# Performance work log

Hardware: AMD Instinct MI355X
Metric: run time of the kernel (lower is better)

Reference implementation:

```python
import jax, jax.numpy as jnp
import numpy as np

VOCAB, E, H, OUT = 24, 16, 32, 2
B, T = 16384, 128


def setup_inputs() -> dict:
    key = jax.random.key(0)
    ks = jax.random.split(key, 8)
    x = jax.random.randint(ks[0], (B, T), 0, VOCAB, dtype=jnp.int32)
    emb = jax.random.normal(ks[1], (VOCAB, E), dtype=jnp.float32) * 0.1
    emb = emb.at[0].set(0.0)  # padding_idx=0
    s = 1.0 / np.sqrt(H)
    W_ih = jax.random.uniform(ks[2], (4 * H, E), minval=-s, maxval=s, dtype=jnp.float32)
    W_hh = jax.random.uniform(ks[3], (4 * H, H), minval=-s, maxval=s, dtype=jnp.float32)
    b_ih = jax.random.uniform(ks[4], (4 * H,), minval=-s, maxval=s, dtype=jnp.float32)
    b_hh = jax.random.uniform(ks[5], (4 * H,), minval=-s, maxval=s, dtype=jnp.float32)
    sf = 1.0 / np.sqrt(H)
    fc_w = jax.random.uniform(ks[6], (OUT, H), minval=-sf, maxval=sf, dtype=jnp.float32)
    fc_b = jax.random.uniform(ks[7], (OUT,), minval=-sf, maxval=sf, dtype=jnp.float32)
    return {"x": x, "emb": emb, "W_ih": W_ih, "W_hh": W_hh,
            "b_ih": b_ih, "b_hh": b_hh, "fc_w": fc_w, "fc_b": fc_b}


def _lstm_last_h(xe, W_ih, W_hh, b_ih, b_hh):
    # xe: [B, T, E]. PyTorch gate order: i, f, g, o.
    b = xe.shape[0]
    # Precompute input projections for all timesteps in one GEMM: [B, T, 4H]
    gates_x = jnp.einsum('bte,ge->btg', xe, W_ih) + (b_ih + b_hh)

    def step(carry, gx_t):
        h, c = carry
        gates = gx_t + h @ W_hh.T  # [B, 4H]
        i, f, g, o = jnp.split(gates, 4, axis=-1)
        i = jax.nn.sigmoid(i)
        f = jax.nn.sigmoid(f)
        g = jnp.tanh(g)
        o = jax.nn.sigmoid(o)
        c = f * c + i * g
        h = o * jnp.tanh(c)
        return (h, c), None

    h0 = jnp.zeros((b, W_hh.shape[1]), dtype=xe.dtype)
    c0 = jnp.zeros_like(h0)
    (h_last, _), _ = jax.lax.scan(step, (h0, c0), jnp.swapaxes(gates_x, 0, 1))
    return h_last  # == lstm_outputs[:, -1, :]


def reference(x, emb, W_ih, W_hh, b_ih, b_hh, fc_w, fc_b):
    xe = emb[x]                                   # [B, T, E] embedding lookup
    h_last = _lstm_last_h(xe, W_ih, W_hh, b_ih, b_hh)  # [B, H]
    return h_last @ fc_w.T + fc_b                 # [B, 2]
```

## Files before the change

kernel.cpp:

```cpp
#include <hip/hip_runtime.h>
#include <hip/hip_bf16.h>

typedef __bf16 bf16x8 __attribute__((ext_vector_type(8)));
typedef float  f32x4  __attribute__((ext_vector_type(4)));

#define VOCAB 24
#define EDIM  16
#define HDIM  32
#define TLEN  128

union A2U { int4 w; bf16x8 v; };

__device__ __forceinline__ float rsig(float a) {
    return __builtin_amdgcn_rcpf(1.0f + __builtin_amdgcn_exp2f(a));
}
__device__ __forceinline__ float fast_tanh(float x) {
    float t = __builtin_amdgcn_exp2f(x * -2.88539008f);
    return fmaf(2.0f, __builtin_amdgcn_rcpf(1.0f + t), -1.0f);
}

__global__ __launch_bounds__(64) void lstm_fused(
    const int*   __restrict__ x,
    const float* __restrict__ emb,
    const float* __restrict__ W_ih,
    const float* __restrict__ W_hh,
    const float* __restrict__ b_ih,
    const float* __restrict__ b_hh,
    const float* __restrict__ fc_w,
    const float* __restrict__ fc_b,
    float*       __restrict__ out)
{
    __shared__ __align__(16) __bf16 hbuf[16][40];
    __shared__ __align__(16) float  fbuf[16][33];

    const int lane  = threadIdx.x;
    const int l15   = lane & 15;
    const int hi    = lane >> 4;
    const int kbase = hi * 8;
    const int kh    = hi * 4;
    const int row0  = blockIdx.x * 16;

    bf16x8 b1f[8];
    bf16x8 b2f[8];
    #pragma unroll
    for (int nt = 0; nt < 8; ++nt) {
        const int gcol = nt * 16 + l15;
        const float scale = ((nt >> 1) == 2) ? -2.88539008f : -1.44269504f;
        const float* wrow = W_hh + gcol * HDIM;
        #pragma unroll
        for (int i = 0; i < 8; ++i)
            b1f[nt][i] = (__bf16)(scale * wrow[kbase + i]);
        const float bias = b_ih[gcol] + b_hh[gcol];
        const float* wi = W_ih + gcol * EDIM;
        #pragma unroll
        for (int i = 0; i < 8; ++i) {
            const int v = kbase + i;
            float s = 0.0f;
            if (v < VOCAB) {
                s = bias;
                #pragma unroll
                for (int e = 0; e < EDIM; ++e)
                    s += emb[v * EDIM + e] * wi[e];
            }
            b2f[nt][i] = (__bf16)(scale * s);
        }
    }

    float c[8];
    #pragma unroll
    for (int q = 0; q < 8; ++q) c[q] = 0.0f;

    f32x4 p[8];
    f32x4 acc[8];
    const f32x4 z = {0.f, 0.f, 0.f, 0.f};
    const int* xrow = x + (row0 + l15) * TLEN;

#define PRECOMP(XV) do {                                                       \
    const int xv_   = (XV);                                                    \
    const int hotw_ = 0x3F80 << ((xv_ & 1) << 4);                              \
    const int hoth_ = xv_ >> 1;                                                \
    A2U a2_;                                                                   \
    a2_.w.x = (hoth_ == kh + 0) ? hotw_ : 0;                                   \
    a2_.w.y = (hoth_ == kh + 1) ? hotw_ : 0;                                   \
    a2_.w.z = (hoth_ == kh + 2) ? hotw_ : 0;                                   \
    a2_.w.w = (hoth_ == kh + 3) ? hotw_ : 0;                                   \
    _Pragma("unroll")                                                          \
    for (int nt = 0; nt < 8; ++nt)                                             \
        p[nt] = __builtin_amdgcn_mfma_f32_16x16x32_bf16(a2_.v, b2f[nt], z, 0, 0, 0); \
} while (0)

#define SLOT(FIRST, LAST, XVN) do {                                            \
    if (FIRST) {                                                               \
        _Pragma("unroll")                                                      \
        for (int nt = 0; nt < 8; ++nt) acc[nt] = p[nt];                        \
    } else {                                                                   \
        const bf16x8 a1_ = *(const bf16x8*)&hbuf[l15][kbase];                  \
        _Pragma("unroll")                                                      \
        for (int nt = 0; nt < 8; ++nt)                                         \
            acc[nt] = __builtin_amdgcn_mfma_f32_16x16x32_bf16(a1_, b1f[nt], p[nt], 0, 0, 0); \
    }                                                                          \
    if (!(LAST)) { PRECOMP(XVN); }        \
    _Pragma("unroll")                                                          \
    for (int qq = 0; qq < 2; ++qq) {                                           \
        _Pragma("unroll")                                                      \
        for (int r = 0; r < 4; ++r) {                                          \
            const float iv = rsig(acc[qq    ][r]);                             \
            const float fv = rsig(acc[qq + 2][r]);                             \
            const float gv = fmaf(2.0f, rsig(acc[qq + 4][r]), -1.0f);          \
            const float ov = rsig(acc[qq + 6][r]);                             \
            c[qq * 4 + r] = fmaf(fv, c[qq * 4 + r], iv * gv);                  \
            const float hv = ov * fast_tanh(c[qq * 4 + r]);                    \
            if (!(LAST)) hbuf[4 * hi + r][qq * 16 + l15] = (__bf16)hv;         \
            else         fbuf[4 * hi + r][qq * 16 + l15] = hv;                 \
        }                                                                      \
    }                                                                          \
} while (0)

    int4 q0 = *(const int4*)xrow;
    int4 xq = *(const int4*)(xrow + 4);
    PRECOMP(q0.x);

    SLOT(true,  false, q0.y);
    SLOT(false, false, q0.z);
    SLOT(false, false, q0.w);
    SLOT(false, false, xq.x);

    #pragma unroll 1
    for (int t = 4; t < 124; t += 4) {
        const int4 n = *(const int4*)(xrow + t + 4);
        SLOT(false, false, xq.y);
        SLOT(false, false, xq.z);
        SLOT(false, false, xq.w);
        SLOT(false, false, n.x);
        xq = n;
    }

    SLOT(false, false, xq.y);
    SLOT(false, false, xq.z);
    SLOT(false, false, xq.w);
    SLOT(false, true,  0);

#undef SLOT
#undef PRECOMP

    __syncthreads();

    if (lane < 16) {
        float o0 = fc_b[0], o1 = fc_b[1];
        #pragma unroll
        for (int jj = 0; jj < HDIM; ++jj) {
            const float h = fbuf[lane][jj];
            o0 += fc_w[jj]        * h;
            o1 += fc_w[HDIM + jj] * h;
        }
        float2 res;
        res.x = o0; res.y = o1;
        *(float2*)&out[(row0 + lane) * 2] = res;
    }
}

extern "C" void kernel_launch(void* const* d_in, const int* in_sizes, int n_in,
                              void* d_out, int out_size, void* d_ws, size_t ws_size,
                              hipStream_t stream) {
    const int*   x    = (const int*)  d_in[0];
    const float* emb  = (const float*)d_in[1];
    const float* W_ih = (const float*)d_in[2];
    const float* W_hh = (const float*)d_in[3];
    const float* b_ih = (const float*)d_in[4];
    const float* b_hh = (const float*)d_in[5];
    const float* fc_w = (const float*)d_in[6];
    const float* fc_b = (const float*)d_in[7];
    float* out = (float*)d_out;

    const int B    = in_sizes[0] / TLEN;
    const int nblk = B / 16;

    lstm_fused<<<nblk, 64, 0, stream>>>(x, emb, W_ih, W_hh, b_ih, b_hh, fc_w, fc_b, out);
}
```

Baseline: 110.1 us.

## Transpose MFMA operands and exchange hidden state via ds_bpermute instead of LDS

```diff
diff --git a/kernel.cpp b/kernel.cpp
--- a/kernel.cpp
+++ b/kernel.cpp
@@ -11,12 +11,12 @@
 
 union A2U { int4 w; bf16x8 v; };
 
-__device__ __forceinline__ float rsig(float a) {
-    return __builtin_amdgcn_rcpf(1.0f + __builtin_amdgcn_exp2f(a));
-}
-__device__ __forceinline__ float fast_tanh(float x) {
-    float t = __builtin_amdgcn_exp2f(x * -2.88539008f);
-    return fmaf(2.0f, __builtin_amdgcn_rcpf(1.0f + t), -1.0f);
+__device__ __forceinline__ float ex2(float x) { return __builtin_amdgcn_exp2f(x); }
+__device__ __forceinline__ float rcpf_(float x) { return __builtin_amdgcn_rcpf(x); }
+__device__ __forceinline__ int cvtpk(float lo, float hi) {
+    int d;
+    asm("v_cvt_pk_bf16_f32 %0, %1, %2" : "=v"(d) : "v"(lo), "v"(hi));
+    return d;
 }
 
 __global__ __launch_bounds__(64) void lstm_fused(
@@ -30,8 +30,7 @@
     const float* __restrict__ fc_b,
     float*       __restrict__ out)
 {
-    __shared__ __align__(16) __bf16 hbuf[16][40];
-    __shared__ __align__(16) float  fbuf[16][33];
+    __shared__ __align__(16) float fbuf[16][33];
 
     const int lane  = threadIdx.x;
     const int l15   = lane & 15;
@@ -75,6 +74,11 @@
     const f32x4 z = {0.f, 0.f, 0.f, 0.f};
     const int* xrow = x + (row0 + l15) * TLEN;
 
+    A2U hb;
+    const int addrA = 4 * (l15 + 32 * (hi & 1));
+    const int addrB = addrA + 64;
+    const bool qsel = (hi >= 2);
+
 #define PRECOMP(XV) do {                                                       \
     const int xv_   = (XV);                                                    \
     const int hotw_ = 0x3F80 << ((xv_ & 1) << 4);                              \
@@ -86,7 +90,7 @@
     a2_.w.w = (hoth_ == kh + 3) ? hotw_ : 0;                                   \
     _Pragma("unroll")                                                          \
     for (int nt = 0; nt < 8; ++nt)                                             \
-        p[nt] = __builtin_amdgcn_mfma_f32_16x16x32_bf16(a2_.v, b2f[nt], z, 0, 0, 0); \
+        p[nt] = __builtin_amdgcn_mfma_f32_16x16x32_bf16(b2f[nt], a2_.v, z, 0, 0, 0); \
 } while (0)
 
 #define SLOT(FIRST, LAST, XVN) do {                                            \
@@ -94,25 +98,48 @@
         _Pragma("unroll")                                                      \
         for (int nt = 0; nt < 8; ++nt) acc[nt] = p[nt];                        \
     } else {                                                                   \
-        const bf16x8 a1_ = *(const bf16x8*)&hbuf[l15][kbase];                  \
         _Pragma("unroll")                                                      \
         for (int nt = 0; nt < 8; ++nt)                                         \
-            acc[nt] = __builtin_amdgcn_mfma_f32_16x16x32_bf16(a1_, b1f[nt], p[nt], 0, 0, 0); \
+            acc[nt] = __builtin_amdgcn_mfma_f32_16x16x32_bf16(b1f[nt], hb.v, p[nt], 0, 0, 0); \
     }                                                                          \
-    if (!(LAST)) { PRECOMP(XVN); }        \
+    float hq[2][4];                                                            \
     _Pragma("unroll")                                                          \
     for (int qq = 0; qq < 2; ++qq) {                                           \
         _Pragma("unroll")                                                      \
-        for (int r = 0; r < 4; ++r) {                                          \
-            const float iv = rsig(acc[qq    ][r]);                             \
-            const float fv = rsig(acc[qq + 2][r]);                             \
-            const float gv = fmaf(2.0f, rsig(acc[qq + 4][r]), -1.0f);          \
-            const float ov = rsig(acc[qq + 6][r]);                             \
-            c[qq * 4 + r] = fmaf(fv, c[qq * 4 + r], iv * gv);                  \
-            const float hv = ov * fast_tanh(c[qq * 4 + r]);                    \
-            if (!(LAST)) hbuf[4 * hi + r][qq * 16 + l15] = (__bf16)hv;         \
-            else         fbuf[4 * hi + r][qq * 16 + l15] = hv;                 \
+        for (int s = 0; s < 4; ++s) {                                          \
+            const float ea = ex2(acc[qq    ][s]);                              \
+            const float ew = ex2(acc[2 + qq][s]);                              \
+            const float eb = ex2(acc[4 + qq][s]);                              \
+            const float ev = ex2(acc[6 + qq][s]);                              \
+            const float R1 = rcpf_(1.0f + ew);                                 \
+            const float R2 = rcpf_((1.0f + ea) * (1.0f + eb));                 \
+            const float cc = fmaf(c[qq * 4 + s], R1, (1.0f - eb) * R2);        \
+            c[qq * 4 + s] = cc;                                                \
+            const float eu = ex2(cc * -2.88539008f);                           \
+            const float R3 = rcpf_((1.0f + ev) * (1.0f + eu));                 \
+            const float hv = (1.0f - eu) * R3;                                 \
+            if (LAST) fbuf[l15][qq * 16 + 4 * hi + s] = hv;                    \
+            else      hq[qq][s] = hv;                                          \
         }                                                                      \
+    }                                                                          \
+    if (!(LAST)) {                                                             \
+        const int PA0 = cvtpk(hq[0][0], hq[0][1]);                             \
+        const int PA1 = cvtpk(hq[0][2], hq[0][3]);                             \
+        const int PB0 = cvtpk(hq[1][0], hq[1][1]);                             \
+        const int PB1 = cvtpk(hq[1][2], hq[1][3]);                             \
+        const int g00 = __builtin_amdgcn_ds_bpermute(addrA, PA0);              \
+        const int g01 = __builtin_amdgcn_ds_bpermute(addrA, PB0);              \
+        const int g10 = __builtin_amdgcn_ds_bpermute(addrA, PA1);              \
+        const int g11 = __builtin_amdgcn_ds_bpermute(addrA, PB1);              \
+        const int g20 = __builtin_amdgcn_ds_bpermute(addrB, PA0);              \
+        const int g21 = __builtin_amdgcn_ds_bpermute(addrB, PB0);              \
+        const int g30 = __builtin_amdgcn_ds_bpermute(addrB, PA1);              \
+        const int g31 = __builtin_amdgcn_ds_bpermute(addrB, PB1);              \
+        hb.w.x = qsel ? g01 : g00;                                             \
+        hb.w.y = qsel ? g11 : g10;                                             \
+        hb.w.z = qsel ? g21 : g20;                                             \
+        hb.w.w = qsel ? g31 : g30;                                             \
+        PRECOMP(XVN);          \
     }                                                                          \
 } while (0)
 
```

New measurement: 117.4 us. +6.7%, slower.

## Halve batch rows per wave and exchange hidden state via DPP and bpermute

Applied to the files above, without the earlier changes.

```diff
diff --git a/kernel.cpp b/kernel.cpp
--- a/kernel.cpp
+++ b/kernel.cpp
@@ -11,15 +11,20 @@
 
 union A2U { int4 w; bf16x8 v; };
 
-__device__ __forceinline__ float rsig(float a) {
-    return __builtin_amdgcn_rcpf(1.0f + __builtin_amdgcn_exp2f(a));
-}
-__device__ __forceinline__ float fast_tanh(float x) {
-    float t = __builtin_amdgcn_exp2f(x * -2.88539008f);
-    return fmaf(2.0f, __builtin_amdgcn_rcpf(1.0f + t), -1.0f);
-}
-
-__global__ __launch_bounds__(64) void lstm_fused(
+__device__ __forceinline__ float ex2(float x)  { return __builtin_amdgcn_exp2f(x); }
+__device__ __forceinline__ float rcpf_(float x){ return __builtin_amdgcn_rcpf(x); }
+__device__ __forceinline__ int cvtpk(float lo, float hi) {
+    int d;
+    asm("v_cvt_pk_bf16_f32 %0, %1, %2" : "=v"(d) : "v"(lo), "v"(hi));
+    return d;
+}
+__device__ __forceinline__ float dpp_upper(float oldv, float srcv) {
+    int r = __builtin_amdgcn_update_dpp(__float_as_int(oldv), __float_as_int(srcv),
+                                        0x128, 0xF, 0xC, false);
+    return __int_as_float(r);
+}
+
+__global__ __launch_bounds__(64, 2) void lstm_fused(
     const int*   __restrict__ x,
     const float* __restrict__ emb,
     const float* __restrict__ W_ih,
@@ -30,15 +35,15 @@
     const float* __restrict__ fc_b,
     float*       __restrict__ out)
 {
-    __shared__ __align__(16) __bf16 hbuf[16][40];
-    __shared__ __align__(16) float  fbuf[16][33];
+    __shared__ __align__(16) float fbuf[8][33];
 
     const int lane  = threadIdx.x;
     const int l15   = lane & 15;
     const int hi    = lane >> 4;
+    const int kh    = hi * 4;
     const int kbase = hi * 8;
-    const int kh    = hi * 4;
-    const int row0  = blockIdx.x * 16;
+    const int row0  = blockIdx.x * 8;
+    const bool lowl = (l15 < 8);
 
     bf16x8 b1f[8];
     bf16x8 b2f[8];
@@ -66,14 +71,21 @@
         }
     }
 
-    float c[8];
+    float c[4];
     #pragma unroll
-    for (int q = 0; q < 8; ++q) c[q] = 0.0f;
+    for (int s = 0; s < 4; ++s) c[s] = 0.0f;
 
     f32x4 p[8];
-    f32x4 acc[8];
     const f32x4 z = {0.f, 0.f, 0.f, 0.f};
-    const int* xrow = x + (row0 + l15) * TLEN;
+    const int* xrow = x + (row0 + (l15 & 7)) * TLEN;
+
+    A2U hb; hb.w.x = hb.w.y = hb.w.z = hb.w.w = 0;
+
+    const int srcA  = ((hi & 1) * 2) * 16 + l15 + 8 * (hi >> 1);
+    const int addrA = 4 * srcA;
+    const int addrB = addrA + 64;
+
+    const int jbase = (lowl ? 0 : 16) + 4 * hi;
 
 #define PRECOMP(XV) do {                                                       \
     const int xv_   = (XV);                                                    \
@@ -86,33 +98,52 @@
     a2_.w.w = (hoth_ == kh + 3) ? hotw_ : 0;                                   \
     _Pragma("unroll")                                                          \
     for (int nt = 0; nt < 8; ++nt)                                             \
-        p[nt] = __builtin_amdgcn_mfma_f32_16x16x32_bf16(a2_.v, b2f[nt], z, 0, 0, 0); \
+        p[nt] = __builtin_amdgcn_mfma_f32_16x16x32_bf16(b2f[nt], a2_.v, z, 0, 0, 0); \
 } while (0)
 
-#define SLOT(FIRST, LAST, XVN) do {                                            \
+#define SLOT(FIRST, LAST, XVN) do {                                           \
+    f32x4 acc_[8];                                                             \
     if (FIRST) {                                                               \
         _Pragma("unroll")                                                      \
-        for (int nt = 0; nt < 8; ++nt) acc[nt] = p[nt];                        \
+        for (int nt = 0; nt < 8; ++nt) acc_[nt] = p[nt];                       \
     } else {                                                                   \
-        const bf16x8 a1_ = *(const bf16x8*)&hbuf[l15][kbase];                  \
         _Pragma("unroll")                                                      \
         for (int nt = 0; nt < 8; ++nt)                                         \
-            acc[nt] = __builtin_amdgcn_mfma_f32_16x16x32_bf16(a1_, b1f[nt], p[nt], 0, 0, 0); \
-    }                                                                          \
-    if (!(LAST)) { PRECOMP(XVN); }        \
+            acc_[nt] = __builtin_amdgcn_mfma_f32_16x16x32_bf16(b1f[nt], hb.v, p[nt], 0, 0, 0); \
+    }                                                                          \
+    float av_[4][4];                                                           \
     _Pragma("unroll")                                                          \
-    for (int qq = 0; qq < 2; ++qq) {                                           \
-        _Pragma("unroll")                                                      \
-        for (int r = 0; r < 4; ++r) {                                          \
-            const float iv = rsig(acc[qq    ][r]);                             \
-            const float fv = rsig(acc[qq + 2][r]);                             \
-            const float gv = fmaf(2.0f, rsig(acc[qq + 4][r]), -1.0f);          \
-            const float ov = rsig(acc[qq + 6][r]);                             \
-            c[qq * 4 + r] = fmaf(fv, c[qq * 4 + r], iv * gv);                  \
-            const float hv = ov * fast_tanh(c[qq * 4 + r]);                    \
-            if (!(LAST)) hbuf[4 * hi + r][qq * 16 + l15] = (__bf16)hv;         \
-            else         fbuf[4 * hi + r][qq * 16 + l15] = hv;                 \
-        }                                                                      \
+    for (int g = 0; g < 4; ++g) {                                              \
+        _Pragma("unroll")                                                      \
+        for (int s = 0; s < 4; ++s)                                            \
+            av_[g][s] = dpp_upper(acc_[2 * g][s], acc_[2 * g + 1][s]);         \
+    }                                                                          \
+    float hv_[4];                                                              \
+    _Pragma("unroll")                                                          \
+    for (int s = 0; s < 4; ++s) {                                              \
+        const float ea = ex2(av_[0][s]);                                \
+        const float ew = ex2(av_[1][s]);                                \
+        const float eb = ex2(av_[2][s]);                     \
+        const float ev = ex2(av_[3][s]);                                \
+        const float R1 = rcpf_(1.0f + ew);                                     \
+        const float R2 = rcpf_((1.0f + ea) * (1.0f + eb));                     \
+        const float cc = fmaf(c[s], R1, (1.0f - eb) * R2);                     \
+        c[s] = cc;                                                             \
+        const float eu = ex2(cc * -2.88539008f);                               \
+        const float R3 = rcpf_((1.0f + ev) * (1.0f + eu));                     \
+        hv_[s] = (1.0f - eu) * R3;                                             \
+    }                                                                          \
+    if (LAST) {                                                                \
+        _Pragma("unroll")                                                      \
+        for (int s = 0; s < 4; ++s) fbuf[l15 & 7][jbase + s] = hv_[s];         \
+    } else {                                                                   \
+        const int w01 = cvtpk(hv_[0], hv_[1]);                                 \
+        const int w23 = cvtpk(hv_[2], hv_[3]);                                 \
+        hb.w.x = __builtin_amdgcn_ds_bpermute(addrA, w01);                     \
+        hb.w.y = __builtin_amdgcn_ds_bpermute(addrA, w23);                     \
+        hb.w.z = __builtin_amdgcn_ds_bpermute(addrB, w01);                     \
+        hb.w.w = __builtin_amdgcn_ds_bpermute(addrB, w23);                     \
+        PRECOMP(XVN);             \
     }                                                                          \
 } while (0)
 
@@ -145,7 +176,7 @@
 
     __syncthreads();
 
-    if (lane < 16) {
+    if (lane < 8) {
         float o0 = fc_b[0], o1 = fc_b[1];
         #pragma unroll
         for (int jj = 0; jj < HDIM; ++jj) {
@@ -173,7 +204,7 @@
     float* out = (float*)d_out;
 
     const int B    = in_sizes[0] / TLEN;
-    const int nblk = B / 16;
+    const int nblk = B / 8;
 
     lstm_fused<<<nblk, 64, 0, stream>>>(x, emb, W_ih, W_hh, b_ih, b_hh, fc_w, fc_b, out);
 }
```

Result: slower. 133.8 us (+21.6%).

## Merge LSTM gate reciprocals algebraically and move h reload after cell update

Applied to the files above, without the earlier changes.

```diff
diff --git a/kernel.cpp b/kernel.cpp
--- a/kernel.cpp
+++ b/kernel.cpp
@@ -11,13 +11,8 @@
 
 union A2U { int4 w; bf16x8 v; };
 
-__device__ __forceinline__ float rsig(float a) {
-    return __builtin_amdgcn_rcpf(1.0f + __builtin_amdgcn_exp2f(a));
-}
-__device__ __forceinline__ float fast_tanh(float x) {
-    float t = __builtin_amdgcn_exp2f(x * -2.88539008f);
-    return fmaf(2.0f, __builtin_amdgcn_rcpf(1.0f + t), -1.0f);
-}
+__device__ __forceinline__ float ex2(float x)  { return __builtin_amdgcn_exp2f(x); }
+__device__ __forceinline__ float rcpf_(float x){ return __builtin_amdgcn_rcpf(x); }
 
 __global__ __launch_bounds__(64) void lstm_fused(
     const int*   __restrict__ x,
@@ -71,7 +66,7 @@
     for (int q = 0; q < 8; ++q) c[q] = 0.0f;
 
     f32x4 p[8];
-    f32x4 acc[8];
+    bf16x8 a1;
     const f32x4 z = {0.f, 0.f, 0.f, 0.f};
     const int* xrow = x + (row0 + l15) * TLEN;
 
@@ -90,29 +85,36 @@
 } while (0)
 
 #define SLOT(FIRST, LAST, XVN) do {                                            \
+    f32x4 acc_[8];                                                             \
     if (FIRST) {                                                               \
         _Pragma("unroll")                                                      \
-        for (int nt = 0; nt < 8; ++nt) acc[nt] = p[nt];                        \
+        for (int nt = 0; nt < 8; ++nt) acc_[nt] = p[nt];                       \
     } else {                                                                   \
-        const bf16x8 a1_ = *(const bf16x8*)&hbuf[l15][kbase];                  \
         _Pragma("unroll")                                                      \
         for (int nt = 0; nt < 8; ++nt)                                         \
-            acc[nt] = __builtin_amdgcn_mfma_f32_16x16x32_bf16(a1_, b1f[nt], p[nt], 0, 0, 0); \
+            acc_[nt] = __builtin_amdgcn_mfma_f32_16x16x32_bf16(a1, b1f[nt], p[nt], 0, 0, 0); \
     }                                                                          \
-    if (!(LAST)) { PRECOMP(XVN); }        \
     _Pragma("unroll")                                                          \
     for (int qq = 0; qq < 2; ++qq) {                                           \
         _Pragma("unroll")                                                      \
         for (int r = 0; r < 4; ++r) {                                          \
-            const float iv = rsig(acc[qq    ][r]);                             \
-            const float fv = rsig(acc[qq + 2][r]);                             \
-            const float gv = fmaf(2.0f, rsig(acc[qq + 4][r]), -1.0f);          \
-            const float ov = rsig(acc[qq + 6][r]);                             \
-            c[qq * 4 + r] = fmaf(fv, c[qq * 4 + r], iv * gv);                  \
-            const float hv = ov * fast_tanh(c[qq * 4 + r]);                    \
+            const float ea = ex2(acc_[qq    ][r]);                      \
+            const float ew = ex2(acc_[qq + 2][r]);                      \
+            const float eb = ex2(acc_[qq + 4][r]);           \
+            const float ev = ex2(acc_[qq + 6][r]);                      \
+            const float P_ = (1.0f + ea) * (1.0f + eb);                        \
+            const float N_ = fmaf(c[qq * 4 + r], P_, (1.0f - eb) * (1.0f + ew)); \
+            const float cc = N_ * rcpf_((1.0f + ew) * P_);                     \
+            c[qq * 4 + r] = cc;                                                \
+            const float eu = ex2(cc * -2.88539008f);                           \
+            const float hv = (1.0f - eu) * rcpf_((1.0f + ev) * (1.0f + eu));   \
             if (!(LAST)) hbuf[4 * hi + r][qq * 16 + l15] = (__bf16)hv;         \
             else         fbuf[4 * hi + r][qq * 16 + l15] = hv;                 \
         }                                                                      \
+    }                                                                          \
+    if (!(LAST)) {                                                             \
+        a1 = *(const bf16x8*)&hbuf[l15][kbase];    \
+        PRECOMP(XVN);             \
     }                                                                          \
 } while (0)
 
```

Measured after the change: 105.1 us. 1.05x faster.
